# Kernel optimization log

Hardware: AMD Instinct MI355X
Metric: run time of the kernel (lower is better)

## Reference

```python
import jax, jax.numpy as jnp
import numpy as np

B, S, H, I, E, R = 2, 2048, 4096, 11008, 4, 8
SCALE = 16.0 / 8.0  # lora_alpha / rank


def _lora(x, A, Bm):
    # x:[N,in], A:[R,in], Bm:[out,R] -> [N,out]
    return (x @ A.T) @ Bm.T * SCALE


def _tmoe(x, router, A, Bm):
    # dense softmax routing over E experts, each a rank-R LoRA
    gates = jax.nn.softmax(x @ router.T, axis=-1)          # [N,E]
    a = jnp.einsum('nh,erh->ner', x, A)                    # [N,E,R]
    return jnp.einsum('ne,ner,eor->no', gates, a, Bm) * SCALE


def _delta(xf, mask, vA, vB, router, tA, tB):
    # image tokens -> V-Adapter LoRA, text tokens -> T-MoE (kd_mode=False)
    return jnp.where(mask[:, None], _lora(xf, vA, vB), _tmoe(xf, router, tA, tB))


def setup_inputs() -> dict:
    key = jax.random.key(0)
    ks = jax.random.split(key, 21)
    w = lambda k, shape: jax.random.normal(k, shape, dtype=jnp.float32) * 0.02
    return {
        'x': jax.random.normal(ks[0], (B, S, H), dtype=jnp.float32) * 0.5,
        'image_mask': jax.random.randint(ks[1], (B, S), 0, 2) == 1,
        'Wg': w(ks[2], (I, H)), 'Wu': w(ks[3], (I, H)), 'Wd': w(ks[4], (H, I)),
        'va_gate_A': w(ks[5], (R, H)), 'va_gate_B': w(ks[6], (I, R)),
        'va_up_A': w(ks[7], (R, H)), 'va_up_B': w(ks[8], (I, R)),
        'va_down_A': w(ks[9], (R, I)), 'va_down_B': w(ks[10], (H, R)),
        'router_gate': w(ks[11], (E, H)), 'tm_gate_A': w(ks[12], (E, R, H)), 'tm_gate_B': w(ks[13], (E, I, R)),
        'router_up': w(ks[14], (E, H)), 'tm_up_A': w(ks[15], (E, R, H)), 'tm_up_B': w(ks[16], (E, I, R)),
        'router_down': w(ks[17], (E, I)), 'tm_down_A': w(ks[18], (E, R, I)), 'tm_down_B': w(ks[19], (E, H, R)),
    }


def reference(x, image_mask, Wg, Wu, Wd,
              va_gate_A, va_gate_B, va_up_A, va_up_B, va_down_A, va_down_B,
              router_gate, tm_gate_A, tm_gate_B,
              router_up, tm_up_A, tm_up_B,
              router_down, tm_down_A, tm_down_B):
    Bb, Ss, Hh = x.shape
    xf = x.reshape(-1, Hh)                                  # [N,H]
    m = image_mask.reshape(-1)                              # [N]
    gate = xf @ Wg.T + _delta(xf, m, va_gate_A, va_gate_B, router_gate, tm_gate_A, tm_gate_B)
    up = xf @ Wu.T + _delta(xf, m, va_up_A, va_up_B, router_up, tm_up_A, tm_up_B)
    inter = jax.nn.silu(gate) * up                          # [N,I]
    out = inter @ Wd.T + _delta(inter, m, va_down_A, va_down_B, router_down, tm_down_A, tm_down_B)
    return out.reshape(Bb, Ss, Hh)
```

## Files before the change

### kernel.cpp

```cpp
#include <hip/hip_runtime.h>
#include <hip/hip_bf16.h>
#include <stdint.h>


#define H_DIM 4096
#define I_DIM 11008
#define N_TOK 4096
#define R_RANK 8
#define K1P 4224
#define K2P 11136

typedef __attribute__((ext_vector_type(8))) __bf16 bf16x8;
typedef __attribute__((ext_vector_type(4))) __bf16 bf16x4;
typedef __attribute__((ext_vector_type(4))) float  f32x4;

__device__ __forceinline__ void gload16(const void* g, const void* lds_wave_base) {
  auto gp = (const __attribute__((address_space(1))) void*)(uintptr_t)g;
  auto lp = (__attribute__((address_space(3))) void*)(uintptr_t)lds_wave_base;
  __builtin_amdgcn_global_load_lds(gp, lp, 16, 0, 0);
}

#define BAR()    asm volatile("s_barrier" ::: "memory")
#define LGKMC(n) do { asm volatile("s_waitcnt lgkmcnt(" #n ")" ::: "memory"); \
                      __builtin_amdgcn_sched_barrier(0); } while (0)
#define SCHEDB() __builtin_amdgcn_sched_barrier(0)

__device__ __forceinline__ void detect_mask(const void* mask, int t, int* okI, int* okF) {
  const unsigned int* mi = (const unsigned int*)mask;
  int bad_i = 0, bad_f = 0;
  for (int idx = t; idx < 1024; idx += 256) {
    unsigned v = mi[idx];
    bad_i |= !(v == 0u || v == 1u);
    bad_f |= !(v == 0u || v == 0x3f800000u);
  }
  if (bad_i) *okI = 0;
  if (bad_f) *okF = 0;
}
__device__ __forceinline__ bool read_mask(const void* mask, int n, int okI, int okF) {
  if (okI) return ((const int*)mask)[n] != 0;
  if (okF) return ((const float*)mask)[n] != 0.0f;
  return ((const unsigned char*)mask)[n] != 0;
}

__global__ __launch_bounds__(256)
void prep_w1(const float* __restrict__ Wg, const float* __restrict__ Wu,
             const float* __restrict__ vBg, const float* __restrict__ tmBg,
             const float* __restrict__ vBu, const float* __restrict__ tmBu,
             __bf16* __restrict__ Wcat) {
  int i = blockIdx.x, t = threadIdx.x;
  int grp = i >> 7, within = i & 127;
  const float4* g4 = (const float4*)(Wg + (size_t)i * H_DIM);
  const float4* u4 = (const float4*)(Wu + (size_t)i * H_DIM);
  __bf16* og = Wcat + (size_t)(grp * 256 + within) * K1P;
  __bf16* ou = Wcat + (size_t)(grp * 256 + 128 + within) * K1P;
  for (int c = t; c < H_DIM / 4; c += 256) {
    float4 v = g4[c];
    bf16x4 b = {(__bf16)v.x, (__bf16)v.y, (__bf16)v.z, (__bf16)v.w};
    *(bf16x4*)(og + c * 4) = b;
    v = u4[c];
    bf16x4 b2 = {(__bf16)v.x, (__bf16)v.y, (__bf16)v.z, (__bf16)v.w};
    *(bf16x4*)(ou + c * 4) = b2;
  }
  if (t < 128) {
    float gv = 0.f, uv = 0.f;
    if (t < 8) gv = 2.f * vBg[i * R_RANK + t];
    else if (t < 40) { int e = (t - 8) >> 3, r = (t - 8) & 7;
      gv = 2.f * tmBg[((size_t)e * I_DIM + i) * R_RANK + r]; }
    if (t >= 40 && t < 48) uv = 2.f * vBu[i * R_RANK + (t - 40)];
    else if (t >= 48 && t < 80) { int e = (t - 48) >> 3, r = (t - 48) & 7;
      uv = 2.f * tmBu[((size_t)e * I_DIM + i) * R_RANK + r]; }
    og[H_DIM + t] = (__bf16)gv;
    ou[H_DIM + t] = (__bf16)uv;
  }
}

__global__ __launch_bounds__(256)
void prep_wd(const float* __restrict__ Wd, const float* __restrict__ vBd,
             const float* __restrict__ tmBd, __bf16* __restrict__ Wda) {
  int o = blockIdx.x, t = threadIdx.x;
  const float4* w4 = (const float4*)(Wd + (size_t)o * I_DIM);
  __bf16* orow = Wda + (size_t)o * K2P;
  for (int c = t; c < I_DIM / 4; c += 256) {
    float4 v = w4[c];
    bf16x4 b = {(__bf16)v.x, (__bf16)v.y, (__bf16)v.z, (__bf16)v.w};
    *(bf16x4*)(orow + c * 4) = b;
  }
  if (t < 128) {
    float v = 0.f;
    if (t < 8) v = 2.f * vBd[o * R_RANK + t];
    else if (t < 40) { int e = (t - 8) >> 3, r = (t - 8) & 7;
      v = 2.f * tmBd[((size_t)e * H_DIM + o) * R_RANK + r]; }
    orow[I_DIM + t] = (__bf16)v;
  }
}

__global__ __launch_bounds__(256)
void prep_x(const float* __restrict__ x, const void* __restrict__ mask,
            const float* __restrict__ vAg, const float* __restrict__ tmAg, const float* __restrict__ rg,
            const float* __restrict__ vAu, const float* __restrict__ tmAu, const float* __restrict__ ru,
            __bf16* __restrict__ Xaug) {
  __shared__ __align__(16) float sx[4][H_DIM];
  __shared__ float dots[4][88];
  __shared__ int okI, okF;
  int t = threadIdx.x, n0 = blockIdx.x * 4;
  if (t == 0) { okI = 1; okF = 1; }
  __syncthreads();
  detect_mask(mask, t, &okI, &okF);
  for (int tok = 0; tok < 4; ++tok) {
    const float4* xr = (const float4*)(x + (size_t)(n0 + tok) * H_DIM);
    __bf16* orow = Xaug + (size_t)(n0 + tok) * K1P;
    for (int c = t; c < H_DIM / 4; c += 256) {
      float4 v = xr[c];
      *(float4*)&sx[tok][c * 4] = v;
      bf16x4 b = {(__bf16)v.x, (__bf16)v.y, (__bf16)v.z, (__bf16)v.w};
      *(bf16x4*)(orow + c * 4) = b;
    }
  }
  __syncthreads();
  int wv = t >> 6, ln = t & 63;
  for (int gi = 0; gi < 6; ++gi) {
    int g = wv + gi * 4;
    if (g >= 22) break;
    int i0 = g * 4;
    const float* base;
    if      (i0 < 8)  base = vAg  + (size_t)i0 * H_DIM;
    else if (i0 < 40) base = tmAg + (size_t)(i0 - 8) * H_DIM;
    else if (i0 < 44) base = rg   + (size_t)(i0 - 40) * H_DIM;
    else if (i0 < 52) base = vAu  + (size_t)(i0 - 44) * H_DIM;
    else if (i0 < 84) base = tmAu + (size_t)(i0 - 52) * H_DIM;
    else              base = ru   + (size_t)(i0 - 84) * H_DIM;
    float acc[4][4];
#pragma unroll
    for (int ii = 0; ii < 4; ++ii)
#pragma unroll
      for (int tk = 0; tk < 4; ++tk) acc[ii][tk] = 0.f;
    for (int j = 0; j < H_DIM / 256; ++j) {
      int h = j * 256 + ln * 4;
      float4 v0 = *(const float4*)&sx[0][h];
      float4 v1 = *(const float4*)&sx[1][h];
      float4 v2 = *(const float4*)&sx[2][h];
      float4 v3 = *(const float4*)&sx[3][h];
#pragma unroll
      for (int ii = 0; ii < 4; ++ii) {
        float4 w = *(const float4*)(base + (size_t)ii * H_DIM + h);
        acc[ii][0] = fmaf(v0.x, w.x, fmaf(v0.y, w.y, fmaf(v0.z, w.z, fmaf(v0.w, w.w, acc[ii][0]))));
        acc[ii][1] = fmaf(v1.x, w.x, fmaf(v1.y, w.y, fmaf(v1.z, w.z, fmaf(v1.w, w.w, acc[ii][1]))));
        acc[ii][2] = fmaf(v2.x, w.x, fmaf(v2.y, w.y, fmaf(v2.z, w.z, fmaf(v2.w, w.w, acc[ii][2]))));
        acc[ii][3] = fmaf(v3.x, w.x, fmaf(v3.y, w.y, fmaf(v3.z, w.z, fmaf(v3.w, w.w, acc[ii][3]))));
      }
    }
#pragma unroll
    for (int ii = 0; ii < 4; ++ii) {
#pragma unroll
      for (int tk = 0; tk < 4; ++tk) {
        float a = acc[ii][tk];
        for (int s = 32; s > 0; s >>= 1) a += __shfl_xor(a, s);
        if (ln == 0) dots[tk][i0 + ii] = a;
      }
    }
  }
  __syncthreads();
  for (int pass = 0; pass < 2; ++pass) {
    int tok = (t >> 7) + pass * 2;
    int s = t & 127;
    const float* dd = dots[tok];
    bool img = read_mask(mask, n0 + tok, okI, okF);
    float c = 0.f;
    if (s < 80) {
      if (s < 40) {
        if (img) { if (s < 8) c = dd[s]; }
        else if (s >= 8) {
          float l0 = dd[40], l1 = dd[41], l2 = dd[42], l3 = dd[43];
          float mx = fmaxf(fmaxf(l0, l1), fmaxf(l2, l3));
          float e0 = __expf(l0 - mx), e1 = __expf(l1 - mx), e2 = __expf(l2 - mx), e3 = __expf(l3 - mx);
          float inv = 1.f / (e0 + e1 + e2 + e3);
          int e = (s - 8) >> 3;
          float ge = (e == 0 ? e0 : e == 1 ? e1 : e == 2 ? e2 : e3) * inv;
          c = ge * dd[s];
        }
      } else {
        int s2 = s - 40;
        if (img) { if (s2 < 8) c = dd[44 + s2]; }
        else if (s2 >= 8) {
          float l0 = dd[84], l1 = dd[85], l2 = dd[86], l3 = dd[87];
          float mx = fmaxf(fmaxf(l0, l1), fmaxf(l2, l3));
          float e0 = __expf(l0 - mx), e1 = __expf(l1 - mx), e2 = __expf(l2 - mx), e3 = __expf(l3 - mx);
          float inv = 1.f / (e0 + e1 + e2 + e3);
          int e = (s2 - 8) >> 3;
          float ge = (e == 0 ? e0 : e == 1 ? e1 : e == 2 ? e2 : e3) * inv;
          c = ge * dd[44 + s2];
        }
      }
    }
    Xaug[(size_t)(n0 + tok) * K1P + H_DIM + s] = (__bf16)c;
  }
}

__global__ __launch_bounds__(512)
void prep_x2(const void* __restrict__ mask, const float* __restrict__ vAd,
             const float* __restrict__ tmAd, const float* __restrict__ rd,
             __bf16* __restrict__ X2) {
  __shared__ __align__(16) __bf16 si[2][I_DIM];
  __shared__ float dots[2][44];
  __shared__ int okI, okF;
  int t = threadIdx.x, n0 = blockIdx.x * 2;
  if (t == 0) { okI = 1; okF = 1; }
  __syncthreads();
  if (t < 256) detect_mask(mask, t, &okI, &okF);
  for (int tok = 0; tok < 2; ++tok) {
    const bf16x8* xr = (const bf16x8*)(X2 + (size_t)(n0 + tok) * K2P);
    bf16x8* srow = (bf16x8*)&si[tok][0];
    for (int c = t; c < I_DIM / 8; c += 512) srow[c] = xr[c];
  }
  __syncthreads();
  int wv = t >> 6, ln = t & 63;
  const bf16x8* s0 = (const bf16x8*)&si[0][0];
  const bf16x8* s1 = (const bf16x8*)&si[1][0];
  for (int gi = 0; gi < 2; ++gi) {
    int g = wv + gi * 8;
    if (g >= 11) break;
    int i0 = g * 4;
    const float* base = (i0 < 8)  ? vAd  + (size_t)i0 * I_DIM
                      : (i0 < 40) ? tmAd + (size_t)(i0 - 8) * I_DIM
                                  : rd   + (size_t)(i0 - 40) * I_DIM;
    float acc[4][2];
#pragma unroll
    for (int ii = 0; ii < 4; ++ii) { acc[ii][0] = 0.f; acc[ii][1] = 0.f; }
    for (int j = 0; j < 22; ++j) {
      int ch = j * 64 + ln;
      if (ch < I_DIM / 8) {
        bf16x8 x0 = s0[ch], x1 = s1[ch];
        float xf0[8], xf1[8];
#pragma unroll
        for (int k = 0; k < 8; ++k) { xf0[k] = (float)x0[k]; xf1[k] = (float)x1[k]; }
#pragma unroll
        for (int ii = 0; ii < 4; ++ii) {
          const float* wrow = base + (size_t)ii * I_DIM;
          float4 wa = *(const float4*)(wrow + ch * 8);
          float4 wb = *(const float4*)(wrow + ch * 8 + 4);
          float a0 = acc[ii][0], a1 = acc[ii][1];
          a0 = fmaf(xf0[0], wa.x, a0); a1 = fmaf(xf1[0], wa.x, a1);
          a0 = fmaf(xf0[1], wa.y, a0); a1 = fmaf(xf1[1], wa.y, a1);
          a0 = fmaf(xf0[2], wa.z, a0); a1 = fmaf(xf1[2], wa.z, a1);
          a0 = fmaf(xf0[3], wa.w, a0); a1 = fmaf(xf1[3], wa.w, a1);
          a0 = fmaf(xf0[4], wb.x, a0); a1 = fmaf(xf1[4], wb.x, a1);
          a0 = fmaf(xf0[5], wb.y, a0); a1 = fmaf(xf1[5], wb.y, a1);
          a0 = fmaf(xf0[6], wb.z, a0); a1 = fmaf(xf1[6], wb.z, a1);
          a0 = fmaf(xf0[7], wb.w, a0); a1 = fmaf(xf1[7], wb.w, a1);
          acc[ii][0] = a0; acc[ii][1] = a1;
        }
      }
    }
#pragma unroll
    for (int ii = 0; ii < 4; ++ii) {
#pragma unroll
      for (int tk = 0; tk < 2; ++tk) {
        float a = acc[ii][tk];
        for (int s = 32; s > 0; s >>= 1) a += __shfl_xor(a, s);
        if (ln == 0) dots[tk][i0 + ii] = a;
      }
    }
  }
  __syncthreads();
  if (t < 256) {
    int tok = t >> 7, s = t & 127;
    const float* dd = dots[tok];
    bool img = read_mask(mask, n0 + tok, okI, okF);
    float c = 0.f;
    if (s < 40) {
      if (img) { if (s < 8) c = dd[s]; }
      else if (s >= 8) {
        float l0 = dd[40], l1 = dd[41], l2 = dd[42], l3 = dd[43];
        float mx = fmaxf(fmaxf(l0, l1), fmaxf(l2, l3));
        float e0 = __expf(l0 - mx), e1 = __expf(l1 - mx), e2 = __expf(l2 - mx), e3 = __expf(l3 - mx);
        float inv = 1.f / (e0 + e1 + e2 + e3);
        int e = (s - 8) >> 3;
        float ge = (e == 0 ? e0 : e == 1 ? e1 : e == 2 ? e2 : e3) * inv;
        c = ge * dd[s];
      }
    }
    X2[(size_t)(n0 + tok) * K2P + I_DIM + s] = (__bf16)c;
  }
}

template<int MH, int NH>
__device__ __forceinline__ void mfmaq(f32x4 (&acc)[8][4], const bf16x8 (&av)[4][2],
                                      const bf16x8 (&bv)[2][2]) {
#pragma unroll
  for (int kk = 0; kk < 2; ++kk)
#pragma unroll
    for (int j = 0; j < 2; ++j)
#pragma unroll
      for (int i = 0; i < 4; ++i)
        acc[MH * 4 + i][NH * 2 + j] = __builtin_amdgcn_mfma_f32_16x16x32_bf16(
            av[i][kk], bv[j][kk], acc[MH * 4 + i][NH * 2 + j], 0, 0, 0);
}

template<int KS, int NT, int GN, typename OutT, int OSTR, int EPI, int MODE>
__global__ __launch_bounds__(512, 2)
void gemm256(const __bf16* __restrict__ A, const __bf16* __restrict__ Bm,
             OutT* __restrict__ C) {
  __shared__ __align__(16) char lds[131072];

  int t = threadIdx.x;
  int w = t >> 6, l = t & 63;
  int wm = w >> 2, wn = w & 3;
  int lrow = l & 15, kq = l >> 4;

  int nwg = gridDim.x, bid = blockIdx.x;
  int tm, tn;
  if constexpr (MODE == 1) {
    int x = bid & 7, i = bid >> 3;
    tm = ((x & 1) << 3) | (i & 7);
    tn = ((x >> 1) << 2) | (i >> 3);
  } else {
    int swz = (bid & 7) * (nwg >> 3) + (bid >> 3);
    tm = swz / GN; tn = swz % GN;
  }
  int m0 = tm * 256, n0 = tn * 256;

  int grow = (t >> 3) & 7;
  int gcole = ((t & 7) ^ grow) << 3;
  const __bf16* gA0 = A  + (size_t)(m0 + w * 8 + grow) * KS + gcole;
  const __bf16* gB0 = Bm + (size_t)(n0 + w * 8 + grow) * KS + gcole;
  char* ldsA0 = lds + w * 1024;
  char* ldsB0 = lds + 32768 + w * 1024;

  auto stageA = [&](int buf, int tt, int c) {
    gload16(gA0 + (size_t)c * (64 * KS) + (size_t)tt * 64,
            ldsA0 + buf * 65536 + c * 8192);
  };
  auto stageB = [&](int buf, int tt, int c) {
    gload16(gB0 + (size_t)c * (64 * KS) + (size_t)tt * 64,
            ldsB0 + buf * 65536 + c * 8192);
  };

  int aBase = (wm * 128 + lrow) * 128;
  int bBase = (wn * 64 + lrow) * 128;
  int sw    = (lrow & 7) << 4;
  int col0  = (kq * 16) ^ sw;
  int col1  = (64 + kq * 16) ^ sw;

  f32x4 acc[8][4];
#pragma unroll
  for (int i = 0; i < 8; ++i)
#pragma unroll
    for (int j = 0; j < 4; ++j) acc[i][j] = (f32x4){0.f, 0.f, 0.f, 0.f};

#pragma unroll
  for (int c = 0; c < 4; ++c) { stageA(0, 0, c); stageB(0, 0, c); }
#pragma unroll
  for (int c = 0; c < 4; ++c) { stageA(1, 1, c); stageB(1, 1, c); }
  asm volatile("s_waitcnt vmcnt(8)" ::: "memory");
  BAR();

  bf16x8 aF[4][2], b0v[2][2], b1v[2][2];
  {
    const char* sb = lds + 32768;
#pragma unroll
    for (int j = 0; j < 2; ++j) {
      b0v[j][0] = *(const bf16x8*)(sb + bBase + j * 2048 + col0);
      b0v[j][1] = *(const bf16x8*)(sb + bBase + j * 2048 + col1);
    }
  }

  int cur = 0;
  for (int tt = 0; tt < NT; ++tt, cur ^= 1) {
    const char* sa  = lds + (cur ? 65536 : 0);
    const char* sb  = sa + 32768;
    const char* sbN = lds + (cur ? 0 : 65536) + 32768;
    int t2 = tt + 2;
    bool st = t2 < NT;

#pragma unroll
    for (int i = 0; i < 4; ++i) {
      aF[i][0] = *(const bf16x8*)(sa + aBase + i * 2048 + col0);
      aF[i][1] = *(const bf16x8*)(sa + aBase + i * 2048 + col1);
    }
    SCHEDB();
#pragma unroll
    for (int j = 0; j < 2; ++j) {
      b1v[j][0] = *(const bf16x8*)(sb + bBase + (2 + j) * 2048 + col0);
      b1v[j][1] = *(const bf16x8*)(sb + bBase + (2 + j) * 2048 + col1);
    }
    BAR(); LGKMC(4);
    __builtin_amdgcn_s_setprio(1);
    mfmaq<0, 0>(acc, aF, b0v);
    __builtin_amdgcn_s_setprio(0);
    BAR();

    if (st) { stageA(cur, t2, 0); stageA(cur, t2, 2); }
    BAR(); LGKMC(0);
    __builtin_amdgcn_s_setprio(1);
    mfmaq<0, 1>(acc, aF, b1v);
    __builtin_amdgcn_s_setprio(0);
    BAR();

    if (st) { stageB(cur, t2, 0); stageB(cur, t2, 1); }
#pragma unroll
    for (int i = 0; i < 4; ++i) {
      aF[i][0] = *(const bf16x8*)(sa + aBase + (4 + i) * 2048 + col0);
      aF[i][1] = *(const bf16x8*)(sa + aBase + (4 + i) * 2048 + col1);
    }
    BAR(); LGKMC(0);
    __builtin_amdgcn_s_setprio(1);
    mfmaq<1, 0>(acc, aF, b0v);
    __builtin_amdgcn_s_setprio(0);
    BAR();

    if (st) { stageB(cur, t2, 2); stageB(cur, t2, 3);
              stageA(cur, t2, 1); stageA(cur, t2, 3); }
    if (st) asm volatile("s_waitcnt vmcnt(8)" ::: "memory");
    else    asm volatile("s_waitcnt vmcnt(0)" ::: "memory");
    SCHEDB();
#pragma unroll
    for (int j = 0; j < 2; ++j) {
      b0v[j][0] = *(const bf16x8*)(sbN + bBase + j * 2048 + col0);
      b0v[j][1] = *(const bf16x8*)(sbN + bBase + j * 2048 + col1);
    }
    BAR(); LGKMC(4);
    __builtin_amdgcn_s_setprio(1);
    mfmaq<1, 1>(acc, aF, b1v);
    __builtin_amdgcn_s_setprio(0);
    BAR();
  }

  if constexpr (EPI == 0) {
    int r0 = m0 + wm * 128 + kq * 4;
    int c0 = n0 + wn * 64 + lrow;
#pragma unroll
    for (int mi = 0; mi < 8; ++mi) {
#pragma unroll
      for (int q = 0; q < 4; ++q) {
        OutT* p = C + (size_t)(r0 + mi * 16 + q) * OSTR + c0;
#pragma unroll
        for (int ni = 0; ni < 4; ++ni) p[ni * 16] = (OutT)acc[mi][ni][q];
      }
    }
  } else {
    float* xch = (float*)lds;
    bool isGate = (wn < 2);
    int p = wm * 2 + (wn & 1);
    float* mybuf = xch + (size_t)p * 8192 + (isGate ? 4096 : 0);
#pragma unroll
    for (int mi = 0; mi < 4; ++mi) {
      int msrc = isGate ? (4 + mi) : mi;
#pragma unroll
      for (int q = 0; q < 4; ++q) {
        int r = mi * 16 + kq * 4 + q;
        int key = (r >> 2) & 3;
#pragma unroll
        for (int ni = 0; ni < 4; ++ni) {
          int c = (ni * 16 + lrow) ^ (key << 4);
          mybuf[r * 64 + c] = acc[msrc][ni][q];
        }
      }
    }
    __syncthreads();
    const float* pbuf = xch + (size_t)p * 8192 + (isGate ? 0 : 4096);
    int mbase = isGate ? 0 : 4;
    int rowoff = isGate ? 0 : 64;
#pragma unroll
    for (int mi = 0; mi < 4; ++mi) {
#pragma unroll
      for (int q = 0; q < 4; ++q) {
        int r = mi * 16 + kq * 4 + q;
        int key = (r >> 2) & 3;
        int row = m0 + wm * 128 + rowoff + r;
        OutT* orow = C + (size_t)row * OSTR + tn * 128 + (wn & 1) * 64 + lrow;
#pragma unroll
        for (int ni = 0; ni < 4; ++ni) {
          int c = (ni * 16 + lrow) ^ (key << 4);
          float o = pbuf[r * 64 + c];
          float g = isGate ? acc[mbase + mi][ni][q] : o;
          float u = isGate ? o : acc[mbase + mi][ni][q];
          orow[ni * 16] = (OutT)(g / (1.f + __expf(-g)) * u);
        }
      }
    }
  }
}

extern "C" void kernel_launch(void* const* d_in, const int* in_sizes, int n_in,
                              void* d_out, int out_size, void* d_ws, size_t ws_size,
                              hipStream_t stream) {
  const float* x    = (const float*)d_in[0];
  const void*  mask = d_in[1];
  const float* Wg   = (const float*)d_in[2];
  const float* Wu   = (const float*)d_in[3];
  const float* Wd   = (const float*)d_in[4];
  const float* vAg  = (const float*)d_in[5];
  const float* vBg  = (const float*)d_in[6];
  const float* vAu  = (const float*)d_in[7];
  const float* vBu  = (const float*)d_in[8];
  const float* vAd  = (const float*)d_in[9];
  const float* vBd  = (const float*)d_in[10];
  const float* rg   = (const float*)d_in[11];
  const float* tmAg = (const float*)d_in[12];
  const float* tmBg = (const float*)d_in[13];
  const float* ru   = (const float*)d_in[14];
  const float* tmAu = (const float*)d_in[15];
  const float* tmBu = (const float*)d_in[16];
  const float* rd   = (const float*)d_in[17];
  const float* tmAd = (const float*)d_in[18];
  const float* tmBd = (const float*)d_in[19];

  char* ws = (char*)d_ws;
  __bf16* Xaug = (__bf16*)(ws);
  __bf16* Wcat = (__bf16*)(ws + 34603008);
  __bf16* X2   = (__bf16*)(ws + 220594176);
  __bf16* Wda  = (__bf16*)(ws + 311820288);

  prep_w1<<<I_DIM, 256, 0, stream>>>(Wg, Wu, vBg, tmBg, vBu, tmBu, Wcat);
  prep_x<<<N_TOK / 4, 256, 0, stream>>>(x, mask, vAg, tmAg, rg, vAu, tmAu, ru, Xaug);

  gemm256<K1P, K1P / 64, 86, __bf16, K2P, 1, 0>
      <<<(N_TOK / 256) * 86, 512, 0, stream>>>(Xaug, Wcat, X2);

  prep_wd<<<H_DIM, 256, 0, stream>>>(Wd, vBd, tmBd, Wda);
  prep_x2<<<N_TOK / 2, 512, 0, stream>>>(mask, vAd, tmAd, rd, X2);

  gemm256<K2P, K2P / 64, H_DIM / 256, float, H_DIM, 0, 1>
      <<<(N_TOK / 256) * (H_DIM / 256), 512, 0, stream>>>(X2, Wda, (float*)d_out);
}
```

Before: 1.668 ms.

## Simplify GEMM LDS fragment schedule and pre-convert LoRA A weights to bf16

The GEMM main loop no longer prefetches the next tile's B fragments across iterations. It loads b0/b1 fragments inside each iteration with full lgkmcnt(0) waits, and issues the last MFMA quarter before the vmcnt wait. A new fused prep kernel converts the LoRA A and router weights to bf16 in scratch areas aliased onto X2 and Wda, so prep_x and prep_x2 read half the bytes. prep_x2 is moved before prep_wd so the aliased Wda space is not overwritten while it is still being read. The GEMM change trades the earlier cross-iteration prefetch for fewer registers and a simpler schedule, but it may expose more LDS latency.

```diff
diff --git a/kernel.cpp b/kernel.cpp
--- a/kernel.cpp
+++ b/kernel.cpp
@@ -20,10 +20,9 @@
   __builtin_amdgcn_global_load_lds(gp, lp, 16, 0, 0);
 }
 
-#define BAR()    asm volatile("s_barrier" ::: "memory")
-#define LGKMC(n) do { asm volatile("s_waitcnt lgkmcnt(" #n ")" ::: "memory"); \
-                      __builtin_amdgcn_sched_barrier(0); } while (0)
-#define SCHEDB() __builtin_amdgcn_sched_barrier(0)
+#define BAR()   asm volatile("s_barrier" ::: "memory")
+#define LGKM0() do { asm volatile("s_waitcnt lgkmcnt(0)" ::: "memory"); \
+                     __builtin_amdgcn_sched_barrier(0); } while (0)
 
 __device__ __forceinline__ void detect_mask(const void* mask, int t, int* okI, int* okF) {
   const unsigned int* mi = (const unsigned int*)mask;
@@ -43,34 +42,66 @@
 }
 
 __global__ __launch_bounds__(256)
-void prep_w1(const float* __restrict__ Wg, const float* __restrict__ Wu,
+void prepAll(const float* __restrict__ Wg, const float* __restrict__ Wu,
              const float* __restrict__ vBg, const float* __restrict__ tmBg,
              const float* __restrict__ vBu, const float* __restrict__ tmBu,
-             __bf16* __restrict__ Wcat) {
-  int i = blockIdx.x, t = threadIdx.x;
-  int grp = i >> 7, within = i & 127;
-  const float4* g4 = (const float4*)(Wg + (size_t)i * H_DIM);
-  const float4* u4 = (const float4*)(Wu + (size_t)i * H_DIM);
-  __bf16* og = Wcat + (size_t)(grp * 256 + within) * K1P;
-  __bf16* ou = Wcat + (size_t)(grp * 256 + 128 + within) * K1P;
-  for (int c = t; c < H_DIM / 4; c += 256) {
-    float4 v = g4[c];
-    bf16x4 b = {(__bf16)v.x, (__bf16)v.y, (__bf16)v.z, (__bf16)v.w};
-    *(bf16x4*)(og + c * 4) = b;
-    v = u4[c];
-    bf16x4 b2 = {(__bf16)v.x, (__bf16)v.y, (__bf16)v.z, (__bf16)v.w};
-    *(bf16x4*)(ou + c * 4) = b2;
-  }
-  if (t < 128) {
-    float gv = 0.f, uv = 0.f;
-    if (t < 8) gv = 2.f * vBg[i * R_RANK + t];
-    else if (t < 40) { int e = (t - 8) >> 3, r = (t - 8) & 7;
-      gv = 2.f * tmBg[((size_t)e * I_DIM + i) * R_RANK + r]; }
-    if (t >= 40 && t < 48) uv = 2.f * vBu[i * R_RANK + (t - 40)];
-    else if (t >= 48 && t < 80) { int e = (t - 48) >> 3, r = (t - 48) & 7;
-      uv = 2.f * tmBu[((size_t)e * I_DIM + i) * R_RANK + r]; }
-    og[H_DIM + t] = (__bf16)gv;
-    ou[H_DIM + t] = (__bf16)uv;
+             const float* __restrict__ vAg, const float* __restrict__ tmAg, const float* __restrict__ rg,
+             const float* __restrict__ vAu, const float* __restrict__ tmAu, const float* __restrict__ ru,
+             const float* __restrict__ vAd, const float* __restrict__ tmAd, const float* __restrict__ rd,
+             __bf16* __restrict__ Wcat, __bf16* __restrict__ W88b, __bf16* __restrict__ W44b) {
+  int b = blockIdx.x, t = threadIdx.x;
+  if (b < I_DIM) {
+    int i = b;
+    int grp = i >> 7, within = i & 127;
+    const float4* g4 = (const float4*)(Wg + (size_t)i * H_DIM);
+    const float4* u4 = (const float4*)(Wu + (size_t)i * H_DIM);
+    __bf16* og = Wcat + (size_t)(grp * 256 + within) * K1P;
+    __bf16* ou = Wcat + (size_t)(grp * 256 + 128 + within) * K1P;
+    for (int c = t; c < H_DIM / 4; c += 256) {
+      float4 v = g4[c];
+      bf16x4 bb = {(__bf16)v.x, (__bf16)v.y, (__bf16)v.z, (__bf16)v.w};
+      *(bf16x4*)(og + c * 4) = bb;
+      v = u4[c];
+      bf16x4 b2 = {(__bf16)v.x, (__bf16)v.y, (__bf16)v.z, (__bf16)v.w};
+      *(bf16x4*)(ou + c * 4) = b2;
+    }
+    if (t < 128) {
+      float gv = 0.f, uv = 0.f;
+      if (t < 8) gv = 2.f * vBg[i * R_RANK + t];
+      else if (t < 40) { int e = (t - 8) >> 3, r = (t - 8) & 7;
+        gv = 2.f * tmBg[((size_t)e * I_DIM + i) * R_RANK + r]; }
+      if (t >= 40 && t < 48) uv = 2.f * vBu[i * R_RANK + (t - 40)];
+      else if (t >= 48 && t < 80) { int e = (t - 48) >> 3, r = (t - 48) & 7;
+        uv = 2.f * tmBu[((size_t)e * I_DIM + i) * R_RANK + r]; }
+      og[H_DIM + t] = (__bf16)gv;
+      ou[H_DIM + t] = (__bf16)uv;
+    }
+  } else if (b < I_DIM + 88) {
+    int r = b - I_DIM;
+    const float* src;
+    if      (r <  8) src = vAg  + (size_t)r * H_DIM;
+    else if (r < 40) src = tmAg + (size_t)(r - 8) * H_DIM;
+    else if (r < 44) src = rg   + (size_t)(r - 40) * H_DIM;
+    else if (r < 52) src = vAu  + (size_t)(r - 44) * H_DIM;
+    else if (r < 84) src = tmAu + (size_t)(r - 52) * H_DIM;
+    else             src = ru   + (size_t)(r - 84) * H_DIM;
+    __bf16* dst = W88b + (size_t)r * H_DIM;
+    for (int c = t; c < H_DIM / 4; c += 256) {
+      float4 v = ((const float4*)src)[c];
+      bf16x4 bb = {(__bf16)v.x, (__bf16)v.y, (__bf16)v.z, (__bf16)v.w};
+      *(bf16x4*)(dst + c * 4) = bb;
+    }
+  } else {
+    int r = b - I_DIM - 88;
+    const float* src = (r < 8)  ? vAd  + (size_t)r * I_DIM
+                     : (r < 40) ? tmAd + (size_t)(r - 8) * I_DIM
+                                : rd   + (size_t)(r - 40) * I_DIM;
+    __bf16* dst = W44b + (size_t)r * I_DIM;
+    for (int c = t; c < I_DIM / 4; c += 256) {
+      float4 v = ((const float4*)src)[c];
+      bf16x4 bb = {(__bf16)v.x, (__bf16)v.y, (__bf16)v.z, (__bf16)v.w};
+      *(bf16x4*)(dst + c * 4) = bb;
+    }
   }
 }
 
@@ -96,9 +127,7 @@
 
 __global__ __launch_bounds__(256)
 void prep_x(const float* __restrict__ x, const void* __restrict__ mask,
-            const float* __restrict__ vAg, const float* __restrict__ tmAg, const float* __restrict__ rg,
-            const float* __restrict__ vAu, const float* __restrict__ tmAu, const float* __restrict__ ru,
-            __bf16* __restrict__ Xaug) {
+            const __bf16* __restrict__ W88b, __bf16* __restrict__ Xaug) {
   __shared__ __align__(16) float sx[4][H_DIM];
   __shared__ float dots[4][88];
   __shared__ int okI, okF;
@@ -122,13 +151,7 @@
     int g = wv + gi * 4;
     if (g >= 22) break;
     int i0 = g * 4;
-    const float* base;
-    if      (i0 < 8)  base = vAg  + (size_t)i0 * H_DIM;
-    else if (i0 < 40) base = tmAg + (size_t)(i0 - 8) * H_DIM;
-    else if (i0 < 44) base = rg   + (size_t)(i0 - 40) * H_DIM;
-    else if (i0 < 52) base = vAu  + (size_t)(i0 - 44) * H_DIM;
-    else if (i0 < 84) base = tmAu + (size_t)(i0 - 52) * H_DIM;
-    else              base = ru   + (size_t)(i0 - 84) * H_DIM;
+    const __bf16* base = W88b + (size_t)i0 * H_DIM;
     float acc[4][4];
 #pragma unroll
     for (int ii = 0; ii < 4; ++ii)
@@ -142,11 +165,12 @@
       float4 v3 = *(const float4*)&sx[3][h];
 #pragma unroll
       for (int ii = 0; ii < 4; ++ii) {
-        float4 w = *(const float4*)(base + (size_t)ii * H_DIM + h);
-        acc[ii][0] = fmaf(v0.x, w.x, fmaf(v0.y, w.y, fmaf(v0.z, w.z, fmaf(v0.w, w.w, acc[ii][0]))));
-        acc[ii][1] = fmaf(v1.x, w.x, fmaf(v1.y, w.y, fmaf(v1.z, w.z, fmaf(v1.w, w.w, acc[ii][1]))));
-        acc[ii][2] = fmaf(v2.x, w.x, fmaf(v2.y, w.y, fmaf(v2.z, w.z, fmaf(v2.w, w.w, acc[ii][2]))));
-        acc[ii][3] = fmaf(v3.x, w.x, fmaf(v3.y, w.y, fmaf(v3.z, w.z, fmaf(v3.w, w.w, acc[ii][3]))));
+        bf16x4 wb = *(const bf16x4*)(base + (size_t)ii * H_DIM + h);
+        float wx = (float)wb[0], wy = (float)wb[1], wz = (float)wb[2], ww = (float)wb[3];
+        acc[ii][0] = fmaf(v0.x, wx, fmaf(v0.y, wy, fmaf(v0.z, wz, fmaf(v0.w, ww, acc[ii][0]))));
+        acc[ii][1] = fmaf(v1.x, wx, fmaf(v1.y, wy, fmaf(v1.z, wz, fmaf(v1.w, ww, acc[ii][1]))));
+        acc[ii][2] = fmaf(v2.x, wx, fmaf(v2.y, wy, fmaf(v2.z, wz, fmaf(v2.w, ww, acc[ii][2]))));
+        acc[ii][3] = fmaf(v3.x, wx, fmaf(v3.y, wy, fmaf(v3.z, wz, fmaf(v3.w, ww, acc[ii][3]))));
       }
     }
 #pragma unroll
@@ -197,8 +221,7 @@
 }
 
 __global__ __launch_bounds__(512)
-void prep_x2(const void* __restrict__ mask, const float* __restrict__ vAd,
-             const float* __restrict__ tmAd, const float* __restrict__ rd,
+void prep_x2(const void* __restrict__ mask, const __bf16* __restrict__ W44b,
              __bf16* __restrict__ X2) {
   __shared__ __align__(16) __bf16 si[2][I_DIM];
   __shared__ float dots[2][44];
@@ -220,9 +243,7 @@
     int g = wv + gi * 8;
     if (g >= 11) break;
     int i0 = g * 4;
-    const float* base = (i0 < 8)  ? vAd  + (size_t)i0 * I_DIM
-                      : (i0 < 40) ? tmAd + (size_t)(i0 - 8) * I_DIM
-                                  : rd   + (size_t)(i0 - 40) * I_DIM;
+    const __bf16* base = W44b + (size_t)i0 * I_DIM;
     float acc[4][2];
 #pragma unroll
     for (int ii = 0; ii < 4; ++ii) { acc[ii][0] = 0.f; acc[ii][1] = 0.f; }
@@ -235,18 +256,14 @@
         for (int k = 0; k < 8; ++k) { xf0[k] = (float)x0[k]; xf1[k] = (float)x1[k]; }
 #pragma unroll
         for (int ii = 0; ii < 4; ++ii) {
-          const float* wrow = base + (size_t)ii * I_DIM;
-          float4 wa = *(const float4*)(wrow + ch * 8);
-          float4 wb = *(const float4*)(wrow + ch * 8 + 4);
+          bf16x8 wv8 = *(const bf16x8*)(base + (size_t)ii * I_DIM + ch * 8);
           float a0 = acc[ii][0], a1 = acc[ii][1];
-          a0 = fmaf(xf0[0], wa.x, a0); a1 = fmaf(xf1[0], wa.x, a1);
-          a0 = fmaf(xf0[1], wa.y, a0); a1 = fmaf(xf1[1], wa.y, a1);
-          a0 = fmaf(xf0[2], wa.z, a0); a1 = fmaf(xf1[2], wa.z, a1);
-          a0 = fmaf(xf0[3], wa.w, a0); a1 = fmaf(xf1[3], wa.w, a1);
-          a0 = fmaf(xf0[4], wb.x, a0); a1 = fmaf(xf1[4], wb.x, a1);
-          a0 = fmaf(xf0[5], wb.y, a0); a1 = fmaf(xf1[5], wb.y, a1);
-          a0 = fmaf(xf0[6], wb.z, a0); a1 = fmaf(xf1[6], wb.z, a1);
-          a0 = fmaf(xf0[7], wb.w, a0); a1 = fmaf(xf1[7], wb.w, a1);
+#pragma unroll
+          for (int k = 0; k < 8; ++k) {
+            float wk = (float)wv8[k];
+            a0 = fmaf(xf0[k], wk, a0);
+            a1 = fmaf(xf1[k], wk, a1);
+          }
           acc[ii][0] = a0; acc[ii][1] = a1;
         }
       }
@@ -354,45 +371,39 @@
   asm volatile("s_waitcnt vmcnt(8)" ::: "memory");
   BAR();
 
-  bf16x8 aF[4][2], b0v[2][2], b1v[2][2];
-  {
-    const char* sb = lds + 32768;
-#pragma unroll
-    for (int j = 0; j < 2; ++j) {
-      b0v[j][0] = *(const bf16x8*)(sb + bBase + j * 2048 + col0);
-      b0v[j][1] = *(const bf16x8*)(sb + bBase + j * 2048 + col1);
-    }
-  }
-
   int cur = 0;
   for (int tt = 0; tt < NT; ++tt, cur ^= 1) {
-    const char* sa  = lds + (cur ? 65536 : 0);
-    const char* sb  = sa + 32768;
-    const char* sbN = lds + (cur ? 0 : 65536) + 32768;
+    const char* sa = lds + (cur ? 65536 : 0);
+    const char* sb = sa + 32768;
     int t2 = tt + 2;
     bool st = t2 < NT;
+    bf16x8 aF[4][2], b0[2][2], b1[2][2];
 
 #pragma unroll
     for (int i = 0; i < 4; ++i) {
       aF[i][0] = *(const bf16x8*)(sa + aBase + i * 2048 + col0);
       aF[i][1] = *(const bf16x8*)(sa + aBase + i * 2048 + col1);
     }
-    SCHEDB();
 #pragma unroll
     for (int j = 0; j < 2; ++j) {
-      b1v[j][0] = *(const bf16x8*)(sb + bBase + (2 + j) * 2048 + col0);
-      b1v[j][1] = *(const bf16x8*)(sb + bBase + (2 + j) * 2048 + col1);
-    }
-    BAR(); LGKMC(4);
+      b0[j][0] = *(const bf16x8*)(sb + bBase + j * 2048 + col0);
+      b0[j][1] = *(const bf16x8*)(sb + bBase + j * 2048 + col1);
+    }
+    BAR(); LGKM0();
     __builtin_amdgcn_s_setprio(1);
-    mfmaq<0, 0>(acc, aF, b0v);
+    mfmaq<0, 0>(acc, aF, b0);
     __builtin_amdgcn_s_setprio(0);
     BAR();
 
     if (st) { stageA(cur, t2, 0); stageA(cur, t2, 2); }
-    BAR(); LGKMC(0);
+#pragma unroll
+    for (int j = 0; j < 2; ++j) {
+      b1[j][0] = *(const bf16x8*)(sb + bBase + (2 + j) * 2048 + col0);
+      b1[j][1] = *(const bf16x8*)(sb + bBase + (2 + j) * 2048 + col1);
+    }
+    BAR(); LGKM0();
     __builtin_amdgcn_s_setprio(1);
-    mfmaq<0, 1>(acc, aF, b1v);
+    mfmaq<0, 1>(acc, aF, b1);
     __builtin_amdgcn_s_setprio(0);
     BAR();
 
@@ -402,26 +413,19 @@
       aF[i][0] = *(const bf16x8*)(sa + aBase + (4 + i) * 2048 + col0);
       aF[i][1] = *(const bf16x8*)(sa + aBase + (4 + i) * 2048 + col1);
     }
-    BAR(); LGKMC(0);
+    BAR(); LGKM0();
     __builtin_amdgcn_s_setprio(1);
-    mfmaq<1, 0>(acc, aF, b0v);
+    mfmaq<1, 0>(acc, aF, b0);
     __builtin_amdgcn_s_setprio(0);
     BAR();
 
     if (st) { stageB(cur, t2, 2); stageB(cur, t2, 3);
               stageA(cur, t2, 1); stageA(cur, t2, 3); }
+    __builtin_amdgcn_s_setprio(1);
+    mfmaq<1, 1>(acc, aF, b1);
+    __builtin_amdgcn_s_setprio(0);
     if (st) asm volatile("s_waitcnt vmcnt(8)" ::: "memory");
     else    asm volatile("s_waitcnt vmcnt(0)" ::: "memory");
-    SCHEDB();
-#pragma unroll
-    for (int j = 0; j < 2; ++j) {
-      b0v[j][0] = *(const bf16x8*)(sbN + bBase + j * 2048 + col0);
-      b0v[j][1] = *(const bf16x8*)(sbN + bBase + j * 2048 + col1);
-    }
-    BAR(); LGKMC(4);
-    __builtin_amdgcn_s_setprio(1);
-    mfmaq<1, 1>(acc, aF, b1v);
-    __builtin_amdgcn_s_setprio(0);
     BAR();
   }
 
@@ -510,15 +514,19 @@
   __bf16* Wcat = (__bf16*)(ws + 34603008);
   __bf16* X2   = (__bf16*)(ws + 220594176);
   __bf16* Wda  = (__bf16*)(ws + 311820288);
-
-  prep_w1<<<I_DIM, 256, 0, stream>>>(Wg, Wu, vBg, tmBg, vBu, tmBu, Wcat);
-  prep_x<<<N_TOK / 4, 256, 0, stream>>>(x, mask, vAg, tmAg, rg, vAu, tmAu, ru, Xaug);
+  __bf16* W88b = X2;
+  __bf16* W44b = Wda;
+
+  prepAll<<<I_DIM + 132, 256, 0, stream>>>(Wg, Wu, vBg, tmBg, vBu, tmBu,
+                                           vAg, tmAg, rg, vAu, tmAu, ru,
+                                           vAd, tmAd, rd, Wcat, W88b, W44b);
+  prep_x<<<N_TOK / 4, 256, 0, stream>>>(x, mask, W88b, Xaug);
 
   gemm256<K1P, K1P / 64, 86, __bf16, K2P, 1, 0>
       <<<(N_TOK / 256) * 86, 512, 0, stream>>>(Xaug, Wcat, X2);
 
+  prep_x2<<<N_TOK / 2, 512, 0, stream>>>(mask, W44b, X2);
   prep_wd<<<H_DIM, 256, 0, stream>>>(Wd, vBd, tmBd, Wda);
-  prep_x2<<<N_TOK / 2, 512, 0, stream>>>(mask, vAd, tmAd, rd, X2);
 
   gemm256<K2P, K2P / 64, H_DIM / 256, float, H_DIM, 0, 1>
       <<<(N_TOK / 256) * (H_DIM / 256), 512, 0, stream>>>(X2, Wda, (float*)d_out);
```

New measurement: 1.458 ms. -12.6%, faster.
